# Kernel optimization log

Hardware: AMD Instinct MI355X
Metric: run time of the kernel (lower is better)

The kernel has to match this reference:

```python
import jax, jax.numpy as jnp
import numpy as np

EPS = 1e-12

def gcn_layer(x, W, row, col, vals, n_nodes):
    # support = x @ W ; out = relu(spmm(adj, support)) with adj in COO form
    support = x @ W                                  # [N, out]
    msgs = vals[:, None] * support[col]              # [E, out] gather
    agg = jax.ops.segment_sum(msgs, row, num_segments=n_nodes)
    return jax.nn.relu(agg)

def l2norm(x):
    return x / jnp.maximum(jnp.linalg.norm(x, axis=1, keepdims=True), EPS)

def setup_inputs() -> dict:
    key = jax.random.key(0)
    ks = jax.random.split(key, 16)
    N, D, A, Da, E = 20000, 1000, 1000, 100, 160000
    inp = {
        'emb_sr': jax.random.normal(ks[0], (N, D), jnp.float32) * 0.02,
        'emb_tg': jax.random.normal(ks[1], (N, D), jnp.float32) * 0.02,
        'attr_weight_sr': jax.random.uniform(ks[2], (N, A), jnp.float32),
        'attr_weight_tg': jax.random.uniform(ks[3], (N, A), jnp.float32),
        'row_sr': jax.random.randint(ks[4], (E,), 0, N, jnp.int32),
        'col_sr': jax.random.randint(ks[5], (E,), 0, N, jnp.int32),
        'vals_sr': jax.random.uniform(ks[6], (E,), jnp.float32),
        'row_tg': jax.random.randint(ks[7], (E,), 0, N, jnp.int32),
        'col_tg': jax.random.randint(ks[8], (E,), 0, N, jnp.int32),
        'vals_tg': jax.random.uniform(ks[9], (E,), jnp.float32),
        'W_s0': jax.random.normal(ks[10], (D, D), jnp.float32) * (1.0 / np.sqrt(D)),
        'W_s1': jax.random.normal(ks[11], (D, D), jnp.float32) * (1.0 / np.sqrt(D)),
        'W_a11': jax.random.normal(ks[12], (A, Da), jnp.float32) * (1.0 / np.sqrt(A)),
        'W_a12': jax.random.normal(ks[13], (A, Da), jnp.float32) * (1.0 / np.sqrt(A)),
        'W_a2': jax.random.normal(ks[14], (Da, Da), jnp.float32) * (1.0 / np.sqrt(Da)),
    }
    return inp

def reference(emb_sr, emb_tg, attr_weight_sr, attr_weight_tg,
              row_sr, col_sr, vals_sr, row_tg, col_tg, vals_tg,
              W_s0, W_s1, W_a11, W_a12, W_a2):
    N = emb_sr.shape[0]
    M = emb_tg.shape[0]
    # structural branch: 2 shared GCN layers over each graph
    sr = emb_sr
    tg = emb_tg
    for W in (W_s0, W_s1):
        sr = gcn_layer(sr, W, row_sr, col_sr, vals_sr, N)
        tg = gcn_layer(tg, W, row_tg, col_tg, vals_tg, M)
    sr = l2norm(sr)
    tg = l2norm(tg)
    # attribute branch
    sr_a = gcn_layer(attr_weight_sr, W_a11, row_sr, col_sr, vals_sr, N)
    sr_a = gcn_layer(sr_a, W_a2, row_sr, col_sr, vals_sr, N)
    tg_a = gcn_layer(attr_weight_tg, W_a12, row_tg, col_tg, vals_tg, M)
    tg_a = gcn_layer(tg_a, W_a2, row_tg, col_tg, vals_tg, M)
    return (sr, tg, sr_a, tg_a)
```

## Files before the change

### kernel.cpp

```cpp
#include <hip/hip_runtime.h>

#define N_NODES 20000
#define D_IN    1000
#define E_EDGES 160000
#define DA      100

#define MPAD 20224
#define DP   1024
#define DAP  128
#define MBLK 157
#define NRB  1250
#define PEMAX (E_EDGES + 4 * N_NODES)

typedef __bf16 bf16x8 __attribute__((ext_vector_type(8)));
typedef float  f32x4  __attribute__((ext_vector_type(4)));
typedef short  short8v __attribute__((ext_vector_type(8)));

__device__ __forceinline__ short f2bf(float f) {
  __bf16 h = (__bf16)f;
  return *(short*)&h;
}
__device__ __forceinline__ float bf2f(short s) {
  return __uint_as_float(((unsigned)(unsigned short)s) << 16);
}

#define GLDS16(g, l) __builtin_amdgcn_global_load_lds( \
    (const __attribute__((address_space(1))) void*)(g), \
    (__attribute__((address_space(3))) void*)(l), 16, 0, 0)


__global__ void cvt_pad4_k(const float* __restrict__ s0, const float* __restrict__ s1,
                           const float* __restrict__ s2, const float* __restrict__ s3,
                           int R, int C,
                           short* __restrict__ d0, short* __restrict__ d1,
                           short* __restrict__ d2, short* __restrict__ d3, int Cp) {
  const float* src; short* dst;
  switch (blockIdx.z) {
    case 0:  src = s0; dst = d0; break;
    case 1:  src = s1; dst = d1; break;
    case 2:  src = s2; dst = d2; break;
    default: src = s3; dst = d3; break;
  }
  int r = blockIdx.y;
  int c0 = threadIdx.x * 4;
  short4 o = {0, 0, 0, 0};
  if (r < R) {
    if (c0 + 3 < C) {
      float4 v = *(const float4*)&src[(size_t)r * C + c0];
      o.x = f2bf(v.x); o.y = f2bf(v.y); o.z = f2bf(v.z); o.w = f2bf(v.w);
    } else {
#pragma unroll
      for (int j = 0; j < 4; ++j) {
        float v = (c0 + j < C) ? src[(size_t)r * C + c0 + j] : 0.f;
        ((short*)&o)[j] = f2bf(v);
      }
    }
  }
  *(short4*)&dst[(size_t)r * Cp + c0] = o;
}

__global__ void cvt_w_t2_k(const float* __restrict__ s0, const float* __restrict__ s1,
                           int K, int Nc,
                           short* __restrict__ d0, short* __restrict__ d1, int Kp) {
  const float* src = blockIdx.z ? s1 : s0;
  short* dst = blockIdx.z ? d1 : d0;
  int n = blockIdx.y;
  int k = blockIdx.x * blockDim.x + threadIdx.x;
  if (k >= Kp) return;
  float v = (k < K && n < Nc) ? src[(size_t)k * Nc + n] : 0.f;
  dst[(size_t)n * Kp + k] = f2bf(v);
}

__global__ void zero_int_k(int* p, int n) {
  int i = blockIdx.x * blockDim.x + threadIdx.x;
  if (i < n) p[i] = 0;
}


__global__ void hist2_k(const int* __restrict__ row0, const int* __restrict__ row1, int E,
                        int* __restrict__ deg0, int* __restrict__ deg1) {
  int e = blockIdx.x * blockDim.x + threadIdx.x;
  if (e < E) atomicAdd(&deg0[row0[e]], 1);
  else if (e < 2 * E) atomicAdd(&deg1[row1[e - E]], 1);
}

#define SCAN_T 1024
#define SCAN_C 20
__launch_bounds__(SCAN_T)
__global__ void scan_pad2_k(const int* __restrict__ dg0, const int* __restrict__ dg1, int n,
                            int* __restrict__ p0, int* __restrict__ p1) {
  const int* deg = blockIdx.x ? dg1 : dg0;
  int* poffs = blockIdx.x ? p1 : p0;
  __shared__ int lds[SCAN_T];
  int t = threadIdx.x;
  int base = t * SCAN_C;
  int v[SCAN_C];
  int s = 0;
#pragma unroll
  for (int i = 0; i < SCAN_C; ++i) {
    int idx = base + i;
    int x = (idx < n) ? ((deg[idx] + 3) & ~3) : 0;
    s += x;
    v[i] = s;
  }
  lds[t] = s;
  __syncthreads();
  for (int off = 1; off < SCAN_T; off <<= 1) {
    int add = (t >= off) ? lds[t - off] : 0;
    __syncthreads();
    lds[t] += add;
    __syncthreads();
  }
  int prefix = lds[t] - s;
#pragma unroll
  for (int i = 0; i < SCAN_C; ++i) {
    int idx = base + i;
    if (idx < n) poffs[idx + 1] = v[i] + prefix;
  }
  if (t == 0) poffs[0] = 0;
}

__global__ void scatter_pack2_k(const int* __restrict__ row0, const int* __restrict__ col0,
                                const float* __restrict__ val0,
                                const int* __restrict__ row1, const int* __restrict__ col1,
                                const float* __restrict__ val1, int E,
                                const int* __restrict__ po0, const int* __restrict__ po1,
                                int* __restrict__ cur0, int* __restrict__ cur1,
                                int2* __restrict__ pk0, int2* __restrict__ pk1) {
  int e = blockIdx.x * blockDim.x + threadIdx.x;
  if (e < E) {
    int r = row0[e];
    int p = atomicAdd(&cur0[r], 1);
    pk0[po0[r] + p] = make_int2(col0[e], __float_as_int(val0[e]));
  } else if (e < 2 * E) {
    int ee = e - E;
    int r = row1[ee];
    int p = atomicAdd(&cur1[r], 1);
    pk1[po1[r] + p] = make_int2(col1[ee], __float_as_int(val1[ee]));
  }
}

__launch_bounds__(512, 1)
__global__ void gemm8p_k(const short* __restrict__ A0, const short* __restrict__ A1, int lda,
                         const short* __restrict__ Bt0, const short* __restrict__ Bt1, int ldb,
                         short* __restrict__ C0, short* __restrict__ C1, int ldc,
                         int nbCol, int nbRow) {
  __shared__ short lds[8][8192];

  int orig = blockIdx.x;
  int nwg = gridDim.x;
  int q = nwg >> 3, rr = nwg & 7;
  int xcd = orig & 7, idx = orig >> 3;
  int wg = (xcd < rr ? xcd * (q + 1) : rr * (q + 1) + (xcd - rr) * q) + idx;
  int colB = wg % nbCol;
  int t2 = wg / nbCol;
  int rowB = t2 % nbRow;
  int z = t2 / nbRow;

  const short* A  = z ? A1 : A0;
  const short* Bt = z ? Bt1 : Bt0;
  short* C        = z ? C1 : C0;

  const int tid  = threadIdx.x;
  const int lane = tid & 63;
  const int wid  = tid >> 6;
  const int wm   = wid >> 2;
  const int wn   = wid & 3;
  const int rowBase = rowB * 256;
  const int colBase = colB * 256;

  const int sC = (lane & 3) ^ ((lane >> 3) & 3);
  const short* baseA = A  + (size_t)(rowBase + wid * 32 + (lane >> 2)) * lda + sC * 8;
  const short* baseB = Bt + (size_t)(colBase + wid * 32 + (lane >> 2)) * ldb + sC * 8;

  const int chunkR = (lane >> 4) ^ ((lane >> 1) & 3);
  const int offA = (wm * 128 + (lane & 15)) * 32 + chunkR * 8;
  const int offB = (wn * 64  + (lane & 15)) * 32 + chunkR * 8;

  f32x4 acc[8][4];
#pragma unroll
  for (int m = 0; m < 8; ++m)
#pragma unroll
    for (int n = 0; n < 4; ++n)
      acc[m][n] = (f32x4){0.f, 0.f, 0.f, 0.f};

#define STAGE_HALF(h) do { \
    int tt_ = (h) >> 2; \
    int kc_ = tt_ * 64 + (((h) >> 1) & 1) * 32; \
    short* dst_ = &lds[(h) & 7][wid * 1024]; \
    if ((h) & 1) { GLDS16(baseB + kc_, dst_); GLDS16(baseB + kc_ + 16 * ldb, dst_ + 512); } \
    else         { GLDS16(baseA + kc_, dst_); GLDS16(baseA + kc_ + 16 * lda, dst_ + 512); } \
  } while (0)

  STAGE_HALF(0); STAGE_HALF(1); STAGE_HALF(2); STAGE_HALF(3); STAGE_HALF(4);
  asm volatile("s_waitcnt vmcnt(6)" ::: "memory");
  __builtin_amdgcn_s_barrier();

  bf16x8 bv[4];
  for (int t = 0; t < 16; ++t) {
    const int s0 = (4 * t) & 7;
    const int s1 = (4 * t + 2) & 7;

    {
      const short* pA = &lds[s0][0];
      const short* pB = &lds[s0 + 1][0];
      bf16x8 af[4];
#pragma unroll
      for (int n = 0; n < 4; ++n) bv[n] = *(const bf16x8*)&pB[offB + n * 512];
#pragma unroll
      for (int m = 0; m < 4; ++m) af[m] = *(const bf16x8*)&pA[offA + m * 512];
      { int h = 4 * t + 5; if (h < 64) STAGE_HALF(h); }
      __builtin_amdgcn_s_barrier();
      __builtin_amdgcn_s_setprio(1);
#pragma unroll
      for (int m = 0; m < 4; ++m)
#pragma unroll
        for (int n = 0; n < 4; ++n)
          acc[m][n] = __builtin_amdgcn_mfma_f32_16x16x32_bf16(af[m], bv[n], acc[m][n], 0, 0, 0);
      __builtin_amdgcn_s_setprio(0);
      __builtin_amdgcn_s_barrier();
    }
    {
      const short* pA = &lds[s0][0];
      bf16x8 af[4];
#pragma unroll
      for (int m = 0; m < 4; ++m) af[m] = *(const bf16x8*)&pA[offA + (4 + m) * 512];
      { int h = 4 * t + 6; if (h < 64) STAGE_HALF(h); }
      __builtin_amdgcn_s_barrier();
      __builtin_amdgcn_s_setprio(1);
#pragma unroll
      for (int m = 0; m < 4; ++m)
#pragma unroll
        for (int n = 0; n < 4; ++n)
          acc[4 + m][n] = __builtin_amdgcn_mfma_f32_16x16x32_bf16(af[m], bv[n], acc[4 + m][n], 0, 0, 0);
      __builtin_amdgcn_s_setprio(0);
      if (t < 15) { asm volatile("s_waitcnt vmcnt(6)" ::: "memory"); }
      else        { asm volatile("s_waitcnt vmcnt(0)" ::: "memory"); }
      __builtin_amdgcn_s_barrier();
    }
    {
      const short* pA = &lds[s1][0];
      const short* pB = &lds[s1 + 1][0];
      bf16x8 af[4];
#pragma unroll
      for (int n = 0; n < 4; ++n) bv[n] = *(const bf16x8*)&pB[offB + n * 512];
#pragma unroll
      for (int m = 0; m < 4; ++m) af[m] = *(const bf16x8*)&pA[offA + m * 512];
      { int h = 4 * t + 7; if (h < 64) STAGE_HALF(h); }
      __builtin_amdgcn_s_barrier();
      __builtin_amdgcn_s_setprio(1);
#pragma unroll
      for (int m = 0; m < 4; ++m)
#pragma unroll
        for (int n = 0; n < 4; ++n)
          acc[m][n] = __builtin_amdgcn_mfma_f32_16x16x32_bf16(af[m], bv[n], acc[m][n], 0, 0, 0);
      __builtin_amdgcn_s_setprio(0);
      __builtin_amdgcn_s_barrier();
    }
    {
      const short* pA = &lds[s1][0];
      bf16x8 af[4];
#pragma unroll
      for (int m = 0; m < 4; ++m) af[m] = *(const bf16x8*)&pA[offA + (4 + m) * 512];
      { int h = 4 * t + 8; if (h < 64) STAGE_HALF(h); }
      __builtin_amdgcn_s_barrier();
      __builtin_amdgcn_s_setprio(1);
#pragma unroll
      for (int m = 0; m < 4; ++m)
#pragma unroll
        for (int n = 0; n < 4; ++n)
          acc[4 + m][n] = __builtin_amdgcn_mfma_f32_16x16x32_bf16(af[m], bv[n], acc[4 + m][n], 0, 0, 0);
      __builtin_amdgcn_s_setprio(0);
      if (t < 14)       { asm volatile("s_waitcnt vmcnt(6)" ::: "memory"); }
      else if (t == 14) { asm volatile("s_waitcnt vmcnt(4)" ::: "memory"); }
      __builtin_amdgcn_s_barrier();
    }
  }
#undef STAGE_HALF

#pragma unroll
  for (int gm = 0; gm < 8; ++gm) {
#pragma unroll
    for (int n = 0; n < 4; ++n) {
      int r0 = rowBase + wm * 128 + gm * 16 + (lane >> 4) * 4;
      int c  = colBase + wn * 64 + n * 16 + (lane & 15);
#pragma unroll
      for (int reg = 0; reg < 4; ++reg)
        C[(size_t)(r0 + reg) * ldc + c] = f2bf(acc[gm][n][reg]);
    }
  }
}

__launch_bounds__(256, 2)
__global__ void gemm_bf16_k(const short* __restrict__ A0, const short* __restrict__ A1, int lda,
                            const short* __restrict__ Bt0, const short* __restrict__ Bt1, int ldb,
                            short* __restrict__ C0, short* __restrict__ C1, int ldc, int K,
                            int nbCol, int nbRow) {
  __shared__ short As[128 * 64];
  __shared__ short Bs[128 * 64];

  int orig = blockIdx.x;
  int nwg = gridDim.x;
  int q = nwg >> 3, rr = nwg & 7;
  int xcd = orig & 7, idx = orig >> 3;
  int wg = (xcd < rr ? xcd * (q + 1) : rr * (q + 1) + (xcd - rr) * q) + idx;
  int colB = wg % nbCol;
  int t2   = wg / nbCol;
  int rowB = t2 % nbRow;
  int z    = t2 / nbRow;

  const short* A  = z ? A1 : A0;
  const short* Bt = z ? Bt1 : Bt0;
  short* C        = z ? C1 : C0;

  const int tid  = threadIdx.x;
  const int lane = tid & 63;
  const int wid  = tid >> 6;
  const int wr   = wid >> 1;
  const int wc   = wid & 1;
  const int rowBase = rowB * 128;
  const int colBase = colB * 128;

  const int lrow = lane >> 3;
  const int kofs = (lane & 7) * 8;

  f32x4 acc[4][4];
#pragma unroll
  for (int m = 0; m < 4; ++m)
#pragma unroll
    for (int n = 0; n < 4; ++n)
      acc[m][n] = (f32x4){0.f, 0.f, 0.f, 0.f};

  for (int k0 = 0; k0 < K; k0 += 64) {
#pragma unroll
    for (int c = 0; c < 4; ++c) {
      int chunk = wid * 4 + c;
      int r = chunk * 8 + lrow;
      const short* g = A + (size_t)(rowBase + r) * lda + k0 + kofs;
      GLDS16(g, &As[chunk * 8 * 64]);
    }
#pragma unroll
    for (int c = 0; c < 4; ++c) {
      int chunk = wid * 4 + c;
      int r = chunk * 8 + lrow;
      const short* g = Bt + (size_t)(colBase + r) * ldb + k0 + kofs;
      GLDS16(g, &Bs[chunk * 8 * 64]);
    }
    __syncthreads();

    bf16x8 af[2][4], bfr[2][4];
#pragma unroll
    for (int kk = 0; kk < 2; ++kk) {
#pragma unroll
      for (int i = 0; i < 4; ++i) {
        int ar = wr * 64 + i * 16 + (lane & 15);
        af[kk][i]  = *(const bf16x8*)&As[ar * 64 + kk * 32 + (lane >> 4) * 8];
        int br = wc * 64 + i * 16 + (lane & 15);
        bfr[kk][i] = *(const bf16x8*)&Bs[br * 64 + kk * 32 + (lane >> 4) * 8];
      }
    }
#pragma unroll
    for (int kk = 0; kk < 2; ++kk)
#pragma unroll
      for (int m = 0; m < 4; ++m)
#pragma unroll
        for (int n = 0; n < 4; ++n)
          acc[m][n] = __builtin_amdgcn_mfma_f32_16x16x32_bf16(
              af[kk][m], bfr[kk][n], acc[m][n], 0, 0, 0);
    __syncthreads();
  }

#pragma unroll
  for (int m = 0; m < 4; ++m) {
#pragma unroll
    for (int n = 0; n < 4; ++n) {
      int row0 = rowBase + wr * 64 + m * 16 + (lane >> 4) * 4;
      int col  = colBase + wc * 64 + n * 16 + (lane & 15);
#pragma unroll
      for (int reg = 0; reg < 4; ++reg)
        C[(size_t)(row0 + reg) * ldc + col] = f2bf(acc[m][n][reg]);
    }
  }
}

template<int NCHUNK, int MODE>
__launch_bounds__(256)
__global__ void spmm_v5(const int* __restrict__ po0, const int* __restrict__ po1,
                        const int2* __restrict__ pk0, const int2* __restrict__ pk1,
                        const short* __restrict__ S0, const short* __restrict__ S1, int ldS,
                        short* __restrict__ oB0, short* __restrict__ oB1, int ldB,
                        float* __restrict__ oF0, float* __restrict__ oF1, int outCols) {
  int orig = blockIdx.x;
  int chunk, graph, rowBlk;
  if (NCHUNK == 8) {
    chunk = orig & 7;
    int idx = orig >> 3;
    graph = idx / NRB;
    rowBlk = idx - graph * NRB;
  } else {
    chunk = 0;
    graph = orig / NRB;
    rowBlk = orig - graph * NRB;
  }
  const int* poffs   = graph ? po1 : po0;
  const int2* packed = graph ? pk1 : pk0;
  const short* S     = graph ? S1 : S0;
  short* outB        = graph ? oB1 : oB0;
  float* outF        = graph ? oF1 : oF0;

  const int lane16 = threadIdx.x & 15;
  const int rowloc = threadIdx.x >> 4;
  const int r  = rowBlk * 16 + rowloc;
  const int c0 = chunk * 128 + lane16 * 8;

  int e0 = poffs[r], e1 = poffs[r + 1];
  float acc[8];
#pragma unroll
  for (int j = 0; j < 8; ++j) acc[j] = 0.f;

  for (int i = e0; i < e1; i += 4) {
    const int4* p4 = (const int4*)&packed[i];
    int4 a = p4[0];
    int4 b = p4[1];
    short8v s0 = *(const short8v*)&S[(size_t)a.x * ldS + c0];
    short8v s1 = *(const short8v*)&S[(size_t)a.z * ldS + c0];
    short8v s2 = *(const short8v*)&S[(size_t)b.x * ldS + c0];
    short8v s3 = *(const short8v*)&S[(size_t)b.z * ldS + c0];
    float v0 = __int_as_float(a.y);
    float v1 = __int_as_float(a.w);
    float v2 = __int_as_float(b.y);
    float v3 = __int_as_float(b.w);
#pragma unroll
    for (int j = 0; j < 8; ++j) {
      acc[j] += v0 * bf2f(s0[j]);
      acc[j] += v1 * bf2f(s1[j]);
      acc[j] += v2 * bf2f(s2[j]);
      acc[j] += v3 * bf2f(s3[j]);
    }
  }
#pragma unroll
  for (int j = 0; j < 8; ++j) acc[j] = fmaxf(acc[j], 0.f);

  if (MODE == 0) {
    short8v o;
#pragma unroll
    for (int j = 0; j < 8; ++j) o[j] = f2bf(acc[j]);
    *(short8v*)&outB[(size_t)r * ldB + c0] = o;
  } else {
#pragma unroll
    for (int j = 0; j < 8; ++j)
      if (c0 + j < outCols)
        outF[(size_t)r * outCols + c0 + j] = acc[j];
  }
}

__launch_bounds__(256)
__global__ void l2norm2_k(const short* __restrict__ H0, const short* __restrict__ H1, int ldH,
                          float* __restrict__ o0, float* __restrict__ o1, int cols) {
  const short* H = blockIdx.y ? H1 : H0;
  float* out = blockIdx.y ? o1 : o0;
  __shared__ float red[4];
  int r = blockIdx.x;
  int t = threadIdx.x;
  short4 v = ((const short4*)(H + (size_t)r * ldH))[t];
  float f0 = bf2f(v.x), f1 = bf2f(v.y), f2 = bf2f(v.z), f3 = bf2f(v.w);
  float s = f0 * f0 + f1 * f1 + f2 * f2 + f3 * f3;
  for (int off = 32; off >= 1; off >>= 1) s += __shfl_down(s, off, 64);
  if ((t & 63) == 0) red[t >> 6] = s;
  __syncthreads();
  float tot = red[0] + red[1] + red[2] + red[3];
  float inv = 1.f / fmaxf(sqrtf(tot), 1e-12f);
  int c0 = t * 4;
  float vals[4] = {f0, f1, f2, f3};
#pragma unroll
  for (int j = 0; j < 4; ++j)
    if (c0 + j < cols)
      out[(size_t)r * cols + c0 + j] = vals[j] * inv;
}


extern "C" void kernel_launch(void* const* d_in, const int* in_sizes, int n_in,
                              void* d_out, int out_size, void* d_ws, size_t ws_size,
                              hipStream_t stream) {
  const float* emb_sr  = (const float*)d_in[0];
  const float* emb_tg  = (const float*)d_in[1];
  const float* attr_sr = (const float*)d_in[2];
  const float* attr_tg = (const float*)d_in[3];
  const int*   row_sr  = (const int*)d_in[4];
  const int*   col_sr  = (const int*)d_in[5];
  const float* vals_sr = (const float*)d_in[6];
  const int*   row_tg  = (const int*)d_in[7];
  const int*   col_tg  = (const int*)d_in[8];
  const float* vals_tg = (const float*)d_in[9];
  const float* W_s0    = (const float*)d_in[10];
  const float* W_s1    = (const float*)d_in[11];
  const float* W_a11   = (const float*)d_in[12];
  const float* W_a12   = (const float*)d_in[13];
  const float* W_a2    = (const float*)d_in[14];

  const int N = N_NODES, Dd = D_IN, E = E_EDGES;

  char* ws = (char*)d_ws;
  size_t off = 0;
  auto alloc = [&](size_t bytes) -> void* {
    void* p = ws + off;
    off += (bytes + 255) & ~(size_t)255;
    return p;
  };
  short* X0 = (short*)alloc((size_t)MPAD * DP * 2);
  short* X1 = (short*)alloc((size_t)MPAD * DP * 2);
  short* T0 = (short*)alloc((size_t)MPAD * DP * 2);
  short* T1 = (short*)alloc((size_t)MPAD * DP * 2);
  short* Y0 = (short*)alloc((size_t)MPAD * DP * 2);
  short* Y1 = (short*)alloc((size_t)MPAD * DP * 2);
  short* Ws0t  = (short*)alloc((size_t)DP * DP * 2);
  short* Ws1t  = (short*)alloc((size_t)DP * DP * 2);
  short* Wa11t = (short*)alloc((size_t)DAP * DP * 2);
  short* Wa12t = (short*)alloc((size_t)DAP * DP * 2);
  short* Wa2t  = (short*)alloc((size_t)DAP * DAP * 2);
  int*  ibuf    = (int*)alloc((size_t)4 * N * 4);
  int2* pack_sr = (int2*)alloc((size_t)PEMAX * 8);
  int2* pack_tg = (int2*)alloc((size_t)PEMAX * 8);
  int*  poffs_sr = (int*)alloc((size_t)(N + 1) * 4);
  int*  poffs_tg = (int*)alloc((size_t)(N + 1) * 4);
  if (off > ws_size) return;

  int* deg_sr = ibuf;
  int* cur_sr = ibuf + N;
  int* deg_tg = ibuf + 2 * N;
  int* cur_tg = ibuf + 3 * N;
  const int ZERO_N = 4 * N + 2 * (PEMAX * 2);

  float* out_sr  = (float*)d_out;
  float* out_tg  = out_sr + (size_t)N * Dd;
  float* out_sra = out_tg + (size_t)N * Dd;
  float* out_tga = out_sra + (size_t)N * DA;

  zero_int_k<<<dim3((ZERO_N + 255) / 256), 256, 0, stream>>>(ibuf, ZERO_N);
  hist2_k<<<dim3((2 * E + 255) / 256), 256, 0, stream>>>(row_sr, row_tg, E, deg_sr, deg_tg);
  scan_pad2_k<<<2, SCAN_T, 0, stream>>>(deg_sr, deg_tg, N, poffs_sr, poffs_tg);
  scatter_pack2_k<<<dim3((2 * E + 255) / 256), 256, 0, stream>>>(
      row_sr, col_sr, vals_sr, row_tg, col_tg, vals_tg, E,
      poffs_sr, poffs_tg, cur_sr, cur_tg, pack_sr, pack_tg);

  cvt_pad4_k<<<dim3(1, MPAD, 4), 256, 0, stream>>>(emb_sr, emb_tg, attr_sr, attr_tg,
                                                   N, Dd, X0, X1, Y0, Y1, DP);
  cvt_w_t2_k<<<dim3(DP / 256, DP, 2), 256, 0, stream>>>(W_s0, W_s1, Dd, Dd, Ws0t, Ws1t, DP);
  cvt_w_t2_k<<<dim3(DP / 256, DAP, 2), 256, 0, stream>>>(W_a11, W_a12, Dd, DA, Wa11t, Wa12t, DP);
  cvt_w_t2_k<<<dim3(1, DAP, 1), 256, 0, stream>>>(W_a2, W_a2, DA, DA, Wa2t, Wa2t, DAP);

  gemm8p_k<<<dim3(79 * 4 * 2), 512, 0, stream>>>(X0, X1, DP, Ws0t, Ws0t, DP,
                                                 T0, T1, DP, 4, 79);
  spmm_v5<8, 0><<<dim3(8 * 2 * NRB), 256, 0, stream>>>(
      poffs_sr, poffs_tg, pack_sr, pack_tg, T0, T1, DP, X0, X1, DP, nullptr, nullptr, 0);
  gemm8p_k<<<dim3(79 * 4 * 2), 512, 0, stream>>>(X0, X1, DP, Ws1t, Ws1t, DP,
                                                 T0, T1, DP, 4, 79);
  spmm_v5<8, 0><<<dim3(8 * 2 * NRB), 256, 0, stream>>>(
      poffs_sr, poffs_tg, pack_sr, pack_tg, T0, T1, DP, X0, X1, DP, nullptr, nullptr, 0);
  l2norm2_k<<<dim3(N, 2), 256, 0, stream>>>(X0, X1, DP, out_sr, out_tg, Dd);

  gemm_bf16_k<<<dim3(1 * MBLK * 2), 256, 0, stream>>>(Y0, Y1, DP, Wa11t, Wa12t, DP,
                                                      T0, T1, DAP, DP, 1, MBLK);
  spmm_v5<1, 0><<<dim3(2 * NRB), 256, 0, stream>>>(
      poffs_sr, poffs_tg, pack_sr, pack_tg, T0, T1, DAP, X0, X1, DAP, nullptr, nullptr, 0);
  gemm_bf16_k<<<dim3(1 * MBLK * 2), 256, 0, stream>>>(X0, X1, DAP, Wa2t, Wa2t, DAP,
                                                      T0, T1, DAP, DAP, 1, MBLK);
  spmm_v5<1, 1><<<dim3(2 * NRB), 256, 0, stream>>>(
      poffs_sr, poffs_tg, pack_sr, pack_tg, T0, T1, DAP, nullptr, nullptr, 0, out_sra, out_tga, DA);
}
```

Baseline: 634.2 us.

## Sort SpMM rows by degree and vectorize the input bf16 conversion

Builds a row permutation that groups rows by degree (clamped to 63) using a counting sort: histogram, scan, then scatter. Each SpMM workgroup then handles 16 rows of similar degree, which reduces load imbalance within a wavefront. The input conversion kernel is also rewritten as a grid-stride loop that writes 8 bf16 values per thread. The cost is three extra small kernels, one extra indirection per row, and output writes that are now scattered instead of contiguous.

```diff
diff --git a/kernel.cpp b/kernel.cpp
--- a/kernel.cpp
+++ b/kernel.cpp
@@ -29,34 +29,30 @@
     (__attribute__((address_space(3))) void*)(l), 16, 0, 0)
 
 
-__global__ void cvt_pad4_k(const float* __restrict__ s0, const float* __restrict__ s1,
-                           const float* __restrict__ s2, const float* __restrict__ s3,
-                           int R, int C,
-                           short* __restrict__ d0, short* __restrict__ d1,
-                           short* __restrict__ d2, short* __restrict__ d3, int Cp) {
-  const float* src; short* dst;
-  switch (blockIdx.z) {
-    case 0:  src = s0; dst = d0; break;
-    case 1:  src = s1; dst = d1; break;
-    case 2:  src = s2; dst = d2; break;
-    default: src = s3; dst = d3; break;
-  }
-  int r = blockIdx.y;
-  int c0 = threadIdx.x * 4;
-  short4 o = {0, 0, 0, 0};
-  if (r < R) {
-    if (c0 + 3 < C) {
-      float4 v = *(const float4*)&src[(size_t)r * C + c0];
-      o.x = f2bf(v.x); o.y = f2bf(v.y); o.z = f2bf(v.z); o.w = f2bf(v.w);
-    } else {
-#pragma unroll
-      for (int j = 0; j < 4; ++j) {
-        float v = (c0 + j < C) ? src[(size_t)r * C + c0 + j] : 0.f;
-        ((short*)&o)[j] = f2bf(v);
-      }
-    }
-  }
-  *(short4*)&dst[(size_t)r * Cp + c0] = o;
+__global__ void cvt_pad4_v2(const float* __restrict__ s0, const float* __restrict__ s1,
+                            const float* __restrict__ s2, const float* __restrict__ s3,
+                            short* __restrict__ d0, short* __restrict__ d1,
+                            short* __restrict__ d2, short* __restrict__ d3) {
+  const int PER = MPAD * 128;
+  const int TOT = 4 * PER;
+  for (int idx = blockIdx.x * blockDim.x + threadIdx.x; idx < TOT;
+       idx += gridDim.x * blockDim.x) {
+    int b = idx / PER;
+    int rem = idx - b * PER;
+    int r = rem >> 7;
+    int g = rem & 127;
+    const float* src = (b == 0) ? s0 : (b == 1) ? s1 : (b == 2) ? s2 : s3;
+    short* dst       = (b == 0) ? d0 : (b == 1) ? d1 : (b == 2) ? d2 : d3;
+    short8v o = {0, 0, 0, 0, 0, 0, 0, 0};
+    if (r < N_NODES && g < 125) {
+      const float* p = src + (size_t)r * D_IN + g * 8;
+      float4 v0 = *(const float4*)p;
+      float4 v1 = *(const float4*)(p + 4);
+      o[0] = f2bf(v0.x); o[1] = f2bf(v0.y); o[2] = f2bf(v0.z); o[3] = f2bf(v0.w);
+      o[4] = f2bf(v1.x); o[5] = f2bf(v1.y); o[6] = f2bf(v1.z); o[7] = f2bf(v1.w);
+    }
+    *(short8v*)&dst[(size_t)r * DP + g * 8] = o;
+  }
 }
 
 __global__ void cvt_w_t2_k(const float* __restrict__ s0, const float* __restrict__ s1,
@@ -140,6 +136,41 @@
   }
 }
 
+__global__ void deghist2_k(const int* __restrict__ deg0, const int* __restrict__ deg1,
+                           int n, int* __restrict__ bins) {
+  int i = blockIdx.x * blockDim.x + threadIdx.x;
+  if (i < n) atomicAdd(&bins[min(deg0[i], 63)], 1);
+  else if (i < 2 * n) atomicAdd(&bins[128 + min(deg1[i - n], 63)], 1);
+}
+
+__global__ void degscan2_k(int* __restrict__ bins) {
+  int t = threadIdx.x;
+  int g = t >> 6, l = t & 63;
+  int v = bins[g * 128 + l];
+  int s = v;
+  for (int off = 1; off < 64; off <<= 1) {
+    int u = __shfl_up(s, off, 64);
+    if (l >= off) s += u;
+  }
+  bins[g * 128 + l] = s - v;
+}
+
+__global__ void degscatter2_k(const int* __restrict__ deg0, const int* __restrict__ deg1,
+                              int n, int* __restrict__ bins,
+                              int* __restrict__ rp0, int* __restrict__ rp1) {
+  int i = blockIdx.x * blockDim.x + threadIdx.x;
+  if (i < n) {
+    int d = min(deg0[i], 63);
+    int p = atomicAdd(&bins[64 + d], 1);
+    rp0[bins[d] + p] = i;
+  } else if (i < 2 * n) {
+    int ii = i - n;
+    int d = min(deg1[ii], 63);
+    int p = atomicAdd(&bins[192 + d], 1);
+    rp1[bins[128 + d] + p] = ii;
+  }
+}
+
 __launch_bounds__(512, 1)
 __global__ void gemm8p_k(const short* __restrict__ A0, const short* __restrict__ A1, int lda,
                          const short* __restrict__ Bt0, const short* __restrict__ Bt1, int ldb,
@@ -385,8 +416,9 @@
 
 template<int NCHUNK, int MODE>
 __launch_bounds__(256)
-__global__ void spmm_v5(const int* __restrict__ po0, const int* __restrict__ po1,
+__global__ void spmm_v6(const int* __restrict__ po0, const int* __restrict__ po1,
                         const int2* __restrict__ pk0, const int2* __restrict__ pk1,
+                        const int* __restrict__ rp0, const int* __restrict__ rp1,
                         const short* __restrict__ S0, const short* __restrict__ S1, int ldS,
                         short* __restrict__ oB0, short* __restrict__ oB1, int ldB,
                         float* __restrict__ oF0, float* __restrict__ oF1, int outCols) {
@@ -404,13 +436,14 @@
   }
   const int* poffs   = graph ? po1 : po0;
   const int2* packed = graph ? pk1 : pk0;
+  const int* rp      = graph ? rp1 : rp0;
   const short* S     = graph ? S1 : S0;
   short* outB        = graph ? oB1 : oB0;
   float* outF        = graph ? oF1 : oF0;
 
   const int lane16 = threadIdx.x & 15;
   const int rowloc = threadIdx.x >> 4;
-  const int r  = rowBlk * 16 + rowloc;
+  const int r  = rp[rowBlk * 16 + rowloc];
   const int c0 = chunk * 128 + lane16 * 8;
 
   int e0 = poffs[r], e1 = poffs[r + 1];
@@ -518,18 +551,21 @@
   short* Wa11t = (short*)alloc((size_t)DAP * DP * 2);
   short* Wa12t = (short*)alloc((size_t)DAP * DP * 2);
   short* Wa2t  = (short*)alloc((size_t)DAP * DAP * 2);
-  int*  ibuf    = (int*)alloc((size_t)4 * N * 4);
+  int*  ibuf    = (int*)alloc(((size_t)4 * N + 256) * 4);
   int2* pack_sr = (int2*)alloc((size_t)PEMAX * 8);
   int2* pack_tg = (int2*)alloc((size_t)PEMAX * 8);
   int*  poffs_sr = (int*)alloc((size_t)(N + 1) * 4);
   int*  poffs_tg = (int*)alloc((size_t)(N + 1) * 4);
+  int*  rperm_sr = (int*)alloc((size_t)N * 4);
+  int*  rperm_tg = (int*)alloc((size_t)N * 4);
   if (off > ws_size) return;
 
   int* deg_sr = ibuf;
   int* cur_sr = ibuf + N;
   int* deg_tg = ibuf + 2 * N;
   int* cur_tg = ibuf + 3 * N;
-  const int ZERO_N = 4 * N + 2 * (PEMAX * 2);
+  int* bins   = ibuf + 4 * N;
+  const int ZERO_N = 4 * N + 256 + 2 * (PEMAX * 2);
 
   float* out_sr  = (float*)d_out;
   float* out_tg  = out_sr + (size_t)N * Dd;
@@ -542,29 +578,37 @@
   scatter_pack2_k<<<dim3((2 * E + 255) / 256), 256, 0, stream>>>(
       row_sr, col_sr, vals_sr, row_tg, col_tg, vals_tg, E,
       poffs_sr, poffs_tg, cur_sr, cur_tg, pack_sr, pack_tg);
-
-  cvt_pad4_k<<<dim3(1, MPAD, 4), 256, 0, stream>>>(emb_sr, emb_tg, attr_sr, attr_tg,
-                                                   N, Dd, X0, X1, Y0, Y1, DP);
+  deghist2_k<<<dim3((2 * N + 255) / 256), 256, 0, stream>>>(deg_sr, deg_tg, N, bins);
+  degscan2_k<<<1, 128, 0, stream>>>(bins);
+  degscatter2_k<<<dim3((2 * N + 255) / 256), 256, 0, stream>>>(deg_sr, deg_tg, N, bins,
+                                                               rperm_sr, rperm_tg);
+
+  cvt_pad4_v2<<<dim3(2048), 256, 0, stream>>>(emb_sr, emb_tg, attr_sr, attr_tg,
+                                              X0, X1, Y0, Y1);
   cvt_w_t2_k<<<dim3(DP / 256, DP, 2), 256, 0, stream>>>(W_s0, W_s1, Dd, Dd, Ws0t, Ws1t, DP);
   cvt_w_t2_k<<<dim3(DP / 256, DAP, 2), 256, 0, stream>>>(W_a11, W_a12, Dd, DA, Wa11t, Wa12t, DP);
   cvt_w_t2_k<<<dim3(1, DAP, 1), 256, 0, stream>>>(W_a2, W_a2, DA, DA, Wa2t, Wa2t, DAP);
 
   gemm8p_k<<<dim3(79 * 4 * 2), 512, 0, stream>>>(X0, X1, DP, Ws0t, Ws0t, DP,
                                                  T0, T1, DP, 4, 79);
-  spmm_v5<8, 0><<<dim3(8 * 2 * NRB), 256, 0, stream>>>(
-      poffs_sr, poffs_tg, pack_sr, pack_tg, T0, T1, DP, X0, X1, DP, nullptr, nullptr, 0);
+  spmm_v6<8, 0><<<dim3(8 * 2 * NRB), 256, 0, stream>>>(
+      poffs_sr, poffs_tg, pack_sr, pack_tg, rperm_sr, rperm_tg,
+      T0, T1, DP, X0, X1, DP, nullptr, nullptr, 0);
   gemm8p_k<<<dim3(79 * 4 * 2), 512, 0, stream>>>(X0, X1, DP, Ws1t, Ws1t, DP,
                                                  T0, T1, DP, 4, 79);
-  spmm_v5<8, 0><<<dim3(8 * 2 * NRB), 256, 0, stream>>>(
-      poffs_sr, poffs_tg, pack_sr, pack_tg, T0, T1, DP, X0, X1, DP, nullptr, nullptr, 0);
+  spmm_v6<8, 0><<<dim3(8 * 2 * NRB), 256, 0, stream>>>(
+      poffs_sr, poffs_tg, pack_sr, pack_tg, rperm_sr, rperm_tg,
+      T0, T1, DP, X0, X1, DP, nullptr, nullptr, 0);
   l2norm2_k<<<dim3(N, 2), 256, 0, stream>>>(X0, X1, DP, out_sr, out_tg, Dd);
 
   gemm_bf16_k<<<dim3(1 * MBLK * 2), 256, 0, stream>>>(Y0, Y1, DP, Wa11t, Wa12t, DP,
                                                       T0, T1, DAP, DP, 1, MBLK);
-  spmm_v5<1, 0><<<dim3(2 * NRB), 256, 0, stream>>>(
-      poffs_sr, poffs_tg, pack_sr, pack_tg, T0, T1, DAP, X0, X1, DAP, nullptr, nullptr, 0);
+  spmm_v6<1, 0><<<dim3(2 * NRB), 256, 0, stream>>>(
+      poffs_sr, poffs_tg, pack_sr, pack_tg, rperm_sr, rperm_tg,
+      T0, T1, DAP, X0, X1, DAP, nullptr, nullptr, 0);
   gemm_bf16_k<<<dim3(1 * MBLK * 2), 256, 0, stream>>>(X0, X1, DAP, Wa2t, Wa2t, DAP,
                                                       T0, T1, DAP, DAP, 1, MBLK);
-  spmm_v5<1, 1><<<dim3(2 * NRB), 256, 0, stream>>>(
-      poffs_sr, poffs_tg, pack_sr, pack_tg, T0, T1, DAP, nullptr, nullptr, 0, out_sra, out_tga, DA);
-}
+  spmm_v6<1, 1><<<dim3(2 * NRB), 256, 0, stream>>>(
+      poffs_sr, poffs_tg, pack_sr, pack_tg, rperm_sr, rperm_tg,
+      T0, T1, DAP, nullptr, nullptr, 0, out_sra, out_tga, DA);
+}
```

After: 790.1 us. +24.6%, slower.
